# Kernel tuning notes

Hardware: AMD Instinct MI355X
Metric: run time of the kernel (lower is better)

## Reference

```python
import jax, jax.numpy as jnp
import numpy as np
import math

EMBED = 256
NH = 8      # num_heads
NP = 4      # num_points
HD = EMBED // NH  # head_dim = 32
BS = 8
NQ = 8192
HH = 128
WW = 128


def setup_inputs() -> dict:
    key = jax.random.key(0)
    ks = jax.random.split(key, 12)
    query = jax.random.normal(ks[0], (BS, NQ, EMBED), jnp.float32)
    reference_points = jax.random.uniform(ks[1], (BS, NQ, 2), dtype=jnp.float32)
    value = jax.random.normal(ks[2], (BS, HH * WW, EMBED), jnp.float32)
    # sampling_offsets: torch init uses zero weight + structured bias (rose pattern);
    # use small random weight so the math path is exercised, keep the structured bias.
    w_off = 0.001 * jax.random.normal(ks[3], (EMBED, NH * NP * 2), jnp.float32)
    thetas = np.arange(NH, dtype=np.float32) * (2.0 * math.pi / NH)
    grid = np.stack([np.cos(thetas), np.sin(thetas)], -1)          # [NH, 2]
    grid = np.tile(grid[:, None, :], (1, NP, 1)) * np.arange(1, NP + 1, dtype=np.float32)[None, :, None]
    b_off = jnp.asarray(grid.reshape(-1), jnp.float32)              # [NH*NP*2]
    w_attn = 0.01 * jax.random.normal(ks[4], (EMBED, NH * NP), jnp.float32)
    b_attn = jnp.zeros((NH * NP,), jnp.float32)
    xav = 1.0 / math.sqrt(EMBED)
    w_val = xav * jax.random.normal(ks[5], (EMBED, EMBED), jnp.float32)
    b_val = jnp.zeros((EMBED,), jnp.float32)
    w_out = xav * jax.random.normal(ks[6], (EMBED, EMBED), jnp.float32)
    b_out = jnp.zeros((EMBED,), jnp.float32)
    return {"query": query, "reference_points": reference_points, "value": value,
            "w_off": w_off, "b_off": b_off, "w_attn": w_attn, "b_attn": b_attn,
            "w_val": w_val, "b_val": b_val, "w_out": w_out, "b_out": b_out,
            "H": HH, "W": WW}


def _deform_attn(query, reference_points, value, w_off, b_off, w_attn, b_attn,
                 w_val, b_val, w_out, b_out, H, W):
    bs, nq, _ = query.shape
    # value projection -> [bs, nh, H*W, hd]
    v = (value @ w_val + b_val).reshape(bs, H * W, NH, HD).transpose(0, 2, 1, 3)
    # offsets and attention weights
    off = (query @ w_off + b_off).reshape(bs, nq, NH, NP, 2)
    attn = jax.nn.softmax((query @ w_attn + b_attn).reshape(bs, nq, NH, NP), axis=-1)
    norm = jnp.array([W, H], dtype=query.dtype)
    loc = reference_points[:, :, None, None, :] + off / norm       # [bs,nq,nh,np,2] in [0,1]
    # grid_sample, align_corners=False: pixel = loc*size - 0.5  (x <-> W, y <-> H)
    px = (loc[..., 0] * W - 0.5).transpose(0, 2, 1, 3).reshape(bs, NH, nq * NP)
    py = (loc[..., 1] * H - 0.5).transpose(0, 2, 1, 3).reshape(bs, NH, nq * NP)
    x0 = jnp.floor(px); y0 = jnp.floor(py)
    wx = px - x0; wy = py - y0
    x0i = x0.astype(jnp.int32); y0i = y0.astype(jnp.int32)

    def gather(xi, yi):
        # padding_mode='zeros': out-of-range corners contribute 0
        mask = ((xi >= 0) & (xi < W) & (yi >= 0) & (yi < H)).astype(v.dtype)
        idx = jnp.clip(yi, 0, H - 1) * W + jnp.clip(xi, 0, W - 1)   # [bs,nh,K]
        g = jnp.take_along_axis(v, idx[..., None], axis=2)          # [bs,nh,K,hd]
        return g * mask[..., None]

    samp = (((1 - wx) * (1 - wy))[..., None] * gather(x0i, y0i)
            + (wx * (1 - wy))[..., None] * gather(x0i + 1, y0i)
            + ((1 - wx) * wy)[..., None] * gather(x0i, y0i + 1)
            + (wx * wy)[..., None] * gather(x0i + 1, y0i + 1))      # [bs,nh,nq*np,hd]
    samp = samp.reshape(bs, NH, nq, NP, HD)
    aw = attn.transpose(0, 2, 1, 3)                                 # [bs,nh,nq,np]
    out = jnp.einsum('bhqpd,bhqp->bqhd', samp, aw).reshape(bs, nq, EMBED)
    return out @ w_out + b_out


def reference(query, reference_points, value, w_off, b_off, w_attn, b_attn,
              w_val, b_val, w_out, b_out, H, W):
    return _deform_attn(query, reference_points, value, w_off, b_off, w_attn, b_attn,
                        w_val, b_val, w_out, b_out, H, W)
```

## Files before the change

### kernel.cpp

```cpp
#include <hip/hip_runtime.h>
#include <stdint.h>

#define NQ 8192
#define BSZ 8
#define NH 8
#define NP 4
#define HD 32
#define EMBED 256
#define IMG 128
#define NPIX (IMG*IMG)

typedef __attribute__((ext_vector_type(8))) short short8v;
typedef __attribute__((ext_vector_type(4))) float f32x4;

static __device__ __forceinline__ float bf2f(uint32_t u) {
    union { uint32_t i; float f; } x; x.i = u << 16; return x.f;
}
static __device__ __forceinline__ uint16_t f2bf(float f) {
    union { float f; uint32_t i; } x; x.f = f;
    uint32_t r = x.i + 0x7fffu + ((x.i >> 16) & 1u);
    return (uint16_t)(r >> 16);
}
static __device__ __forceinline__ uint32_t cvtpk(float lo, float hi) {
    uint32_t r;
    asm("v_cvt_pk_bf16_f32 %0, %1, %2" : "=v"(r) : "v"(lo), "v"(hi));
    return r;
}
static __device__ __forceinline__ void gload_lds16(const void* g, void* l) {
    __builtin_amdgcn_global_load_lds(
        (const __attribute__((address_space(1))) unsigned int*)g,
        (__attribute__((address_space(3))) unsigned int*)l, 16, 0, 0);
}

#define WAITV(n) asm volatile("s_waitcnt vmcnt(" #n ")" ::: "memory")
#define BARRIER() do { __builtin_amdgcn_s_barrier(); \
                       __builtin_amdgcn_sched_barrier(0); } while (0)

__global__ void pack_w(const float* __restrict__ w_val, const float* __restrict__ w_out,
                       const float* __restrict__ w_off, const float* __restrict__ w_attn,
                       uint16_t* __restrict__ wTval, uint16_t* __restrict__ wTout,
                       uint16_t* __restrict__ wTcat) {
    int k = blockIdx.x;
    int n = threadIdx.x;
    wTval[n * 256 + k] = f2bf(w_val[k * 256 + n]);
    wTout[n * 256 + k] = f2bf(w_out[k * 256 + n]);
    if (n < 64)       wTcat[n * 256 + k]        = f2bf(w_off[k * 64 + n]);
    else if (n < 96)  wTcat[n * 256 + k]        = f2bf(w_attn[k * 32 + (n - 64)]);
}

template<bool A_F32, bool OUT_F32, bool PLANE>
__global__ __launch_bounds__(256, 1)
void gemm_k256(const void* __restrict__ Ap, const uint16_t* __restrict__ BT,
               void* __restrict__ Cp, const float* __restrict__ bias, int M) {
    constexpr int ABYTES = A_F32 ? 16384 : 8192;
    __shared__ char SMEM[131072 + 2 * ABYTES];
    char* Bs = SMEM;
    char* Adbuf[2] = { SMEM + 131072, SMEM + 131072 + ABYTES };
    const int tid = threadIdx.x;
    const int w = tid >> 6, l = tid & 63;
    const int bm = blockIdx.x;
    const int wc = w * 64;

    auto stageA = [&](int buf, int s) {
        const int rowg0 = bm * 64 + s * 16;
        if constexpr (A_F32) {
#pragma unroll
            for (int c = 0; c < 4; ++c) {
                int row = c * 4 + w;
                int x = l * 16;
                const char* src = (const char*)Ap + (size_t)(rowg0 + row) * 1024
                                  + (x ^ ((row & 7) << 4));
                gload_lds16(src, Adbuf[buf] + row * 1024);
            }
        } else {
#pragma unroll
            for (int c = 0; c < 2; ++c) {
                int row2 = (c * 4 + w) * 2;
                int row = row2 + (l >> 5);
                int x = (l & 31) * 16;
                const char* src = (const char*)Ap + (size_t)(rowg0 + row) * 512
                                  + (x ^ ((row & 7) << 4));
                gload_lds16(src, Adbuf[buf] + row2 * 512);
            }
        }
    };

#pragma unroll
    for (int c = 0; c < 32; ++c) {
        int loff = c * 4096 + w * 1024;
        int lofl = loff + l * 16;
        int row = lofl >> 9, x = lofl & 511;
        const char* src = (const char*)BT + (size_t)row * 512 + (x ^ ((row & 7) << 4));
        gload_lds16(src, Bs + loff);
    }
    stageA(0, 0);
    stageA(1, 1);
    if constexpr (A_F32) { WAITV(8); } else { WAITV(4); }
    BARRIER();

    short8v breg[4][8];
#pragma unroll
    for (int n = 0; n < 4; ++n) {
        int col = wc + n * 16 + (l & 15);
        const char* base = Bs + col * 512;
        const int sz = (col & 7) << 4;
#pragma unroll
        for (int k = 0; k < 8; ++k)
            breg[n][k] = *(const short8v*)(base + ((k * 64 + (l >> 4) * 16) ^ sz));
    }

    f32x4 acc[4][4] = {};

#pragma unroll
    for (int s = 0; s < 4; ++s) {
        if (s == 3)              { WAITV(0); }
        else if constexpr (A_F32){ WAITV(4); }
        else                     { WAITV(2); }
        BARRIER();
        const int buf = s & 1;
        short8v a[8];
        const int sz = (l & 7) << 4;
        if constexpr (A_F32) {
            const char* base = Adbuf[buf] + (l & 15) * 1024;
#pragma unroll
            for (int k = 0; k < 8; ++k) {
                int off = k * 128 + (l >> 4) * 32;
                f32x4 lo = *(const f32x4*)(base + (off ^ sz));
                f32x4 hi = *(const f32x4*)(base + ((off + 16) ^ sz));
                union { uint32_t u[4]; short8v s8; } pk;
                pk.u[0] = cvtpk(lo[0], lo[1]); pk.u[1] = cvtpk(lo[2], lo[3]);
                pk.u[2] = cvtpk(hi[0], hi[1]); pk.u[3] = cvtpk(hi[2], hi[3]);
                a[k] = pk.s8;
            }
        } else {
            const char* base = Adbuf[buf] + (l & 15) * 512;
#pragma unroll
            for (int k = 0; k < 8; ++k)
                a[k] = *(const short8v*)(base + ((k * 64 + (l >> 4) * 16) ^ sz));
        }
#pragma unroll
        for (int k = 0; k < 8; ++k)
#pragma unroll
            for (int n = 0; n < 4; ++n)
                acc[s][n] = __builtin_amdgcn_mfma_f32_16x16x32_bf16(a[k], breg[n][k], acc[s][n], 0, 0, 0);
        BARRIER();
        if (s < 2) stageA(buf, s + 2);
    }

    if constexpr (PLANE) {
        uint16_t* Cs = (uint16_t*)(SMEM + 131072);
#pragma unroll
        for (int s = 0; s < 4; ++s)
#pragma unroll
            for (int n = 0; n < 4; ++n) {
                int lcol = wc + n * 16 + (l & 15);
                float bv = bias[lcol];
#pragma unroll
                for (int r = 0; r < 4; ++r) {
                    int lrow = s * 16 + (l >> 4) * 4 + r;
                    *(uint16_t*)((char*)Cs + ((lrow * 512 + lcol * 2) ^ ((lrow & 7) << 4)))
                        = f2bf(acc[s][n][r] + bv);
                }
            }
        __syncthreads();
#pragma unroll
        for (int i = 0; i < 8; ++i) {
            int byteoff = i * 4096 + tid * 16;
            int lrow = byteoff >> 9, x = byteoff & 511;
            uint4 d = *(const uint4*)((const char*)Cs + ((lrow * 512 + x) ^ ((lrow & 7) << 4)));
            int lcol = x >> 1;
            int gr = bm * 64 + lrow;
            int b_ = gr >> 14, pix = gr & 16383;
            int h_ = lcol >> 5, d_ = lcol & 31;
            *(uint4*)((char*)Cp + (((size_t)(b_ * 8 + h_)) << 20) + (size_t)pix * 64 + d_ * 2) = d;
        }
    } else {
#pragma unroll
        for (int s = 0; s < 4; ++s)
#pragma unroll
            for (int n = 0; n < 4; ++n) {
                int col = wc + n * 16 + (l & 15);
                float bv = bias[col];
#pragma unroll
                for (int r = 0; r < 4; ++r) {
                    int gr = bm * 64 + s * 16 + (l >> 4) * 4 + r;
                    float val = acc[s][n][r] + bv;
                    if constexpr (OUT_F32)
                        ((float*)Cp)[(size_t)gr * 256 + col] = val;
                    else
                        ((uint16_t*)Cp)[(size_t)gr * 256 + col] = f2bf(val);
                }
            }
    }
}

__global__ __launch_bounds__(256, 2)
void proj_kernel(const float* __restrict__ Q, const uint16_t* __restrict__ WTcat,
                 const float* __restrict__ b_off, const float* __restrict__ b_attn,
                 const float* __restrict__ refp,
                 float* __restrict__ locs, float* __restrict__ attnw) {
    __shared__ uint16_t Bs[96 * 256];
    __shared__ uint16_t As[64 * 256];
    const int tid = threadIdx.x, w = tid >> 6, l = tid & 63;
    const int blk = blockIdx.x;

#pragma unroll
    for (int c = 0; c < 12; ++c) {
        int loff = (w * 12 + c) * 1024;
        int lofl = loff + l * 16;
        int row = lofl >> 9, colb = lofl & 511;
        const char* src = (const char*)WTcat + (size_t)row * 512 + (colb ^ ((row & 7) << 4));
        gload_lds16(src, (char*)Bs + loff);
    }
#pragma unroll
    for (int c = 0; c < 8; ++c) {
        int loff = tid * 16 + c * 4096;
        int row = loff >> 9, colb = loff & 511;
        const float* src = Q + (size_t)(blk * 64 + row) * 256 + (colb >> 1);
        float4 f0 = *(const float4*)src;
        float4 f1 = *(const float4*)(src + 4);
        uint4 pk;
        pk.x = (uint32_t)f2bf(f0.x) | ((uint32_t)f2bf(f0.y) << 16);
        pk.y = (uint32_t)f2bf(f0.z) | ((uint32_t)f2bf(f0.w) << 16);
        pk.z = (uint32_t)f2bf(f1.x) | ((uint32_t)f2bf(f1.y) << 16);
        pk.w = (uint32_t)f2bf(f1.z) | ((uint32_t)f2bf(f1.w) << 16);
        *(uint4*)((char*)As + row * 512 + (colb ^ ((row & 7) << 4))) = pk;
    }
    __syncthreads();

    f32x4 acc[6] = {};
    const int arow = w * 16 + (l & 15);
#pragma unroll
    for (int ks = 0; ks < 8; ++ks) {
        const int kb = ks * 64 + (l >> 4) * 16;
        short8v a = *(const short8v*)((const char*)As + arow * 512 + (kb ^ ((arow & 7) << 4)));
#pragma unroll
        for (int n = 0; n < 6; ++n) {
            int col = n * 16 + (l & 15);
            short8v b = *(const short8v*)((const char*)Bs + col * 512 + (kb ^ ((col & 7) << 4)));
            acc[n] = __builtin_amdgcn_mfma_f32_16x16x32_bf16(a, b, acc[n], 0, 0, 0);
        }
    }
    __syncthreads();
    float* scores = (float*)As;
#pragma unroll
    for (int n = 0; n < 6; ++n)
#pragma unroll
        for (int r = 0; r < 4; ++r)
            scores[(w * 16 + (l >> 4) * 4 + r) * 96 + n * 16 + (l & 15)] = acc[n][r];
    __syncthreads();

    for (int it = tid; it < 512; it += 256) {
        int row = it >> 3, h = it & 7;
        int gq = blk * 64 + row;
        int b = gq >> 13, q = gq & 8191;
        size_t itemH = ((size_t)(b * 8 + h) << 13) | q;
        float s0 = scores[row * 96 + 64 + h * 4 + 0] + b_attn[h * 4 + 0];
        float s1 = scores[row * 96 + 64 + h * 4 + 1] + b_attn[h * 4 + 1];
        float s2 = scores[row * 96 + 64 + h * 4 + 2] + b_attn[h * 4 + 2];
        float s3 = scores[row * 96 + 64 + h * 4 + 3] + b_attn[h * 4 + 3];
        float mx = fmaxf(fmaxf(s0, s1), fmaxf(s2, s3));
        float e0 = __expf(s0 - mx), e1 = __expf(s1 - mx);
        float e2 = __expf(s2 - mx), e3 = __expf(s3 - mx);
        float inv = 1.0f / (e0 + e1 + e2 + e3);
        float rx = refp[gq * 2 + 0] * 128.0f - 0.5f;
        float ry = refp[gq * 2 + 1] * 128.0f - 0.5f;
        float ew[4] = { e0, e1, e2, e3 };
#pragma unroll
        for (int p = 0; p < 4; ++p) {
            float ox = scores[row * 96 + h * 8 + p * 2 + 0] + b_off[h * 8 + p * 2 + 0];
            float oy = scores[row * 96 + h * 8 + p * 2 + 1] + b_off[h * 8 + p * 2 + 1];
            locs[itemH * 8 + p * 2 + 0] = rx + ox;
            locs[itemH * 8 + p * 2 + 1] = ry + oy;
            attnw[itemH * 4 + p] = ew[p] * inv;
        }
    }
}

__global__ __launch_bounds__(256)
void sample_kernel(const uint16_t* __restrict__ v, const float* __restrict__ locs,
                   const float* __restrict__ attnw, uint16_t* __restrict__ oatt) {
    const int bid = blockIdx.x;
    const int h = bid & 7;
    const int rest = bid >> 3;
    const int b = rest >> 7;
    const int chunk = rest & 127;
    const int qloc = threadIdx.x >> 2;
    const int dg = threadIdx.x & 3;
    const int q = chunk * 64 + qloc;
    const size_t itemH = ((size_t)(b * 8 + h) << 13) | q;
    const char* plane = (const char*)v + ((size_t)(b * 8 + h) << 20);

    float4 l01 = ((const float4*)locs)[itemH * 2 + 0];
    float4 l23 = ((const float4*)locs)[itemH * 2 + 1];
    float4 aw4 = ((const float4*)attnw)[itemH];
    float pxs[4] = { l01.x, l01.z, l23.x, l23.z };
    float pys[4] = { l01.y, l01.w, l23.y, l23.w };
    float aws[4] = { aw4.x, aw4.y, aw4.z, aw4.w };

    float acc[8] = {};
#pragma unroll
    for (int p = 0; p < 4; ++p) {
        float px = pxs[p], py = pys[p], aw = aws[p];
        float fx = floorf(px), fy = floorf(py);
        float wx = px - fx, wy = py - fy;
        int x0 = (int)fx, y0 = (int)fy;
#pragma unroll
        for (int cy = 0; cy < 2; ++cy) {
            int yy = y0 + cy;
            float wyv = cy ? wy : 1.f - wy;
            bool yok = (unsigned)yy < (unsigned)IMG;
            int yc = min(max(yy, 0), IMG - 1);
#pragma unroll
            for (int cx = 0; cx < 2; ++cx) {
                int xx = x0 + cx;
                bool ok = yok && ((unsigned)xx < (unsigned)IMG);
                int xc = min(max(xx, 0), IMG - 1);
                float wgt = ok ? aw * (cx ? wx : 1.f - wx) * wyv : 0.f;
                const uint4 u = *(const uint4*)(plane + ((size_t)(yc * IMG + xc) << 6) + dg * 16);
                acc[0] += wgt * bf2f(u.x & 0xffffu);
                acc[1] += wgt * bf2f(u.x >> 16);
                acc[2] += wgt * bf2f(u.y & 0xffffu);
                acc[3] += wgt * bf2f(u.y >> 16);
                acc[4] += wgt * bf2f(u.z & 0xffffu);
                acc[5] += wgt * bf2f(u.z >> 16);
                acc[6] += wgt * bf2f(u.w & 0xffffu);
                acc[7] += wgt * bf2f(u.w >> 16);
            }
        }
    }
    const size_t bq = (size_t)b * NQ + q;
    uint4 out;
    out.x = (uint32_t)f2bf(acc[0]) | ((uint32_t)f2bf(acc[1]) << 16);
    out.y = (uint32_t)f2bf(acc[2]) | ((uint32_t)f2bf(acc[3]) << 16);
    out.z = (uint32_t)f2bf(acc[4]) | ((uint32_t)f2bf(acc[5]) << 16);
    out.w = (uint32_t)f2bf(acc[6]) | ((uint32_t)f2bf(acc[7]) << 16);
    *(uint4*)((char*)oatt + (bq * 256 + h * 32 + dg * 8) * 2) = out;
}

extern "C" void kernel_launch(void* const* d_in, const int* in_sizes, int n_in,
                              void* d_out, int out_size, void* d_ws, size_t ws_size,
                              hipStream_t stream) {
    const float* query  = (const float*)d_in[0];
    const float* refp   = (const float*)d_in[1];
    const float* value  = (const float*)d_in[2];
    const float* w_off  = (const float*)d_in[3];
    const float* b_off  = (const float*)d_in[4];
    const float* w_attn = (const float*)d_in[5];
    const float* b_attn = (const float*)d_in[6];
    const float* w_val  = (const float*)d_in[7];
    const float* b_val  = (const float*)d_in[8];
    const float* w_out  = (const float*)d_in[9];
    const float* b_out  = (const float*)d_in[10];

    char* ws = (char*)d_ws;
    uint16_t* v     = (uint16_t*)(ws);
    uint16_t* oatt  = (uint16_t*)(ws + 67108864);
    float*    locs  = (float*)(ws + 100663296);
    float*    attnw = (float*)(ws + 117440512);
    uint16_t* wTval = (uint16_t*)(ws + 125829120);
    uint16_t* wTout = (uint16_t*)(ws + 125960192);
    uint16_t* wTcat = (uint16_t*)(ws + 126091264);

    pack_w<<<256, 256, 0, stream>>>(w_val, w_out, w_off, w_attn, wTval, wTout, wTcat);
    gemm_k256<true, false, true><<<2048, 256, 0, stream>>>(value, wTval, v, b_val, 131072);
    proj_kernel<<<1024, 256, 0, stream>>>(query, wTcat, b_off, b_attn, refp, locs, attnw);
    sample_kernel<<<8192, 256, 0, stream>>>(v, locs, attnw, oatt);
    gemm_k256<false, true, false><<<1024, 256, 0, stream>>>(oatt, wTout, (float*)d_out, b_out, 65536);
}
```

Before: 154.9 us.

## Make projection GEMMs persistent over stripes with a deeper A-tile ring buffer

Replaces the one-stripe-per-block GEMM with a 512-thread kernel in which each block handles several 64-row stripes. The 128KB weight tile is loaded into LDS and registers once per block instead of once per stripe. The A-operand pipeline grows from double buffering to a ring with six loads in flight, so global loads overlap MFMA work across stripes. In exchange each block now uses about 160KB of LDS and more registers, so at most one block fits per CU. The grid also becomes 256 blocks, which can leave load imbalance with little room to hide latency.

```diff
diff --git a/kernel.cpp b/kernel.cpp
--- a/kernel.cpp
+++ b/kernel.cpp
@@ -33,8 +33,20 @@
 }
 
 #define WAITV(n) asm volatile("s_waitcnt vmcnt(" #n ")" ::: "memory")
+#define WAITLGKM() do { asm volatile("s_waitcnt lgkmcnt(0)" ::: "memory"); \
+                        __builtin_amdgcn_sched_barrier(0); } while (0)
 #define BARRIER() do { __builtin_amdgcn_s_barrier(); \
                        __builtin_amdgcn_sched_barrier(0); } while (0)
+
+static __device__ __forceinline__ void waitv_n(int n) {
+    switch (n) {
+        case 0: WAITV(0); break;  case 1: WAITV(1); break;
+        case 2: WAITV(2); break;  case 3: WAITV(3); break;
+        case 4: WAITV(4); break;  case 5: WAITV(5); break;
+        case 6: WAITV(6); break;  case 8: WAITV(8); break;
+        default: WAITV(10); break;
+    }
+}
 
 __global__ void pack_w(const float* __restrict__ w_val, const float* __restrict__ w_out,
                        const float* __restrict__ w_off, const float* __restrict__ w_attn,
@@ -48,149 +60,146 @@
     else if (n < 96)  wTcat[n * 256 + k]        = f2bf(w_attn[k * 32 + (n - 64)]);
 }
 
-template<bool A_F32, bool OUT_F32, bool PLANE>
-__global__ __launch_bounds__(256, 1)
-void gemm_k256(const void* __restrict__ Ap, const uint16_t* __restrict__ BT,
-               void* __restrict__ Cp, const float* __restrict__ bias, int M) {
-    constexpr int ABYTES = A_F32 ? 16384 : 8192;
-    __shared__ char SMEM[131072 + 2 * ABYTES];
-    char* Bs = SMEM;
-    char* Adbuf[2] = { SMEM + 131072, SMEM + 131072 + ABYTES };
-    const int tid = threadIdx.x;
-    const int w = tid >> 6, l = tid & 63;
-    const int bm = blockIdx.x;
-    const int wc = w * 64;
-
-    auto stageA = [&](int buf, int s) {
-        const int rowg0 = bm * 64 + s * 16;
+template<bool A_F32, bool OUT_F32, bool PLANE, int STRIPES>
+__global__ __launch_bounds__(512, 2)
+void gemm_pk(const void* __restrict__ Ap, const uint16_t* __restrict__ BT,
+             void* __restrict__ Cp, const float* __restrict__ bias) {
+    constexpr int TILEB = A_F32 ? 16384 : 8192;
+    constexpr int NR    = 131072 / TILEB;
+    constexpr int T     = STRIPES * 4;
+    constexpr int LPT   = A_F32 ? 2 : 1;
+    __shared__ char SMEM[131072 + (PLANE ? 32768 : 0)];
+    char* ring = SMEM;
+    const int tid = threadIdx.x, w = tid >> 6, l = tid & 63;
+    const int stripe0 = blockIdx.x * STRIPES;
+
+    auto stageA = [&](int slot, int t) {
+        const int gr0 = (stripe0 + (t >> 2)) * 64 + (t & 3) * 16;
         if constexpr (A_F32) {
 #pragma unroll
-            for (int c = 0; c < 4; ++c) {
-                int row = c * 4 + w;
-                int x = l * 16;
-                const char* src = (const char*)Ap + (size_t)(rowg0 + row) * 1024
+            for (int c = 0; c < 2; ++c) {
+                int loff = c * 8192 + tid * 16;
+                int row = loff >> 10, x = loff & 1023;
+                const char* src = (const char*)Ap + (size_t)(gr0 + row) * 1024
                                   + (x ^ ((row & 7) << 4));
-                gload_lds16(src, Adbuf[buf] + row * 1024);
+                gload_lds16(src, ring + slot * 16384 + c * 8192 + w * 1024);
             }
         } else {
-#pragma unroll
-            for (int c = 0; c < 2; ++c) {
-                int row2 = (c * 4 + w) * 2;
-                int row = row2 + (l >> 5);
-                int x = (l & 31) * 16;
-                const char* src = (const char*)Ap + (size_t)(rowg0 + row) * 512
-                                  + (x ^ ((row & 7) << 4));
-                gload_lds16(src, Adbuf[buf] + row2 * 512);
-            }
+            int loff = tid * 16;
+            int row = loff >> 9, x = loff & 511;
+            const char* src = (const char*)Ap + (size_t)(gr0 + row) * 512
+                              + (x ^ ((row & 7) << 4));
+            gload_lds16(src, ring + slot * 8192 + w * 1024);
         }
     };
 
 #pragma unroll
-    for (int c = 0; c < 32; ++c) {
-        int loff = c * 4096 + w * 1024;
-        int lofl = loff + l * 16;
-        int row = lofl >> 9, x = lofl & 511;
+    for (int c = 0; c < 16; ++c) {
+        int loff = c * 8192 + tid * 16;
+        int row = loff >> 9, x = loff & 511;
         const char* src = (const char*)BT + (size_t)row * 512 + (x ^ ((row & 7) << 4));
-        gload_lds16(src, Bs + loff);
-    }
-    stageA(0, 0);
-    stageA(1, 1);
-    if constexpr (A_F32) { WAITV(8); } else { WAITV(4); }
+        gload_lds16(src, SMEM + c * 8192 + w * 1024);
+    }
+    WAITV(0);
     BARRIER();
-
-    short8v breg[4][8];
-#pragma unroll
-    for (int n = 0; n < 4; ++n) {
-        int col = wc + n * 16 + (l & 15);
-        const char* base = Bs + col * 512;
+    short8v breg[2][8];
+#pragma unroll
+    for (int n = 0; n < 2; ++n) {
+        int col = w * 32 + n * 16 + (l & 15);
+        const char* base = SMEM + col * 512;
         const int sz = (col & 7) << 4;
 #pragma unroll
         for (int k = 0; k < 8; ++k)
             breg[n][k] = *(const short8v*)(base + ((k * 64 + (l >> 4) * 16) ^ sz));
     }
-
-    f32x4 acc[4][4] = {};
-
-#pragma unroll
-    for (int s = 0; s < 4; ++s) {
-        if (s == 3)              { WAITV(0); }
-        else if constexpr (A_F32){ WAITV(4); }
-        else                     { WAITV(2); }
-        BARRIER();
-        const int buf = s & 1;
-        short8v a[8];
-        const int sz = (l & 7) << 4;
-        if constexpr (A_F32) {
-            const char* base = Adbuf[buf] + (l & 15) * 1024;
-#pragma unroll
-            for (int k = 0; k < 8; ++k) {
-                int off = k * 128 + (l >> 4) * 32;
-                f32x4 lo = *(const f32x4*)(base + (off ^ sz));
-                f32x4 hi = *(const f32x4*)(base + ((off + 16) ^ sz));
-                union { uint32_t u[4]; short8v s8; } pk;
-                pk.u[0] = cvtpk(lo[0], lo[1]); pk.u[1] = cvtpk(lo[2], lo[3]);
-                pk.u[2] = cvtpk(hi[0], hi[1]); pk.u[3] = cvtpk(hi[2], hi[3]);
-                a[k] = pk.s8;
+    WAITLGKM();
+    BARRIER();
+#pragma unroll
+    for (int t = 0; t < 6; ++t) stageA(t & (NR - 1), t);
+
+    for (int st = 0; st < STRIPES; ++st) {
+        f32x4 acc[4][2] = {};
+#pragma unroll
+        for (int s = 0; s < 4; ++s) {
+            const int t = st * 4 + s;
+            const int rem = T - 1 - t;
+            waitv_n((rem < 5 ? rem : 5) * LPT);
+            BARRIER();
+            if (t + 6 < T) stageA((t + 6) & (NR - 1), t + 6);
+            const int slot = t & (NR - 1);
+            short8v a[8];
+            const int sz = (l & 7) << 4;
+            if constexpr (A_F32) {
+                const char* base = ring + slot * 16384 + (l & 15) * 1024;
+#pragma unroll
+                for (int k = 0; k < 8; ++k) {
+                    int off = k * 128 + (l >> 4) * 32;
+                    f32x4 lo = *(const f32x4*)(base + (off ^ sz));
+                    f32x4 hi = *(const f32x4*)(base + ((off + 16) ^ sz));
+                    union { uint32_t u[4]; short8v s8; } pk;
+                    pk.u[0] = cvtpk(lo[0], lo[1]); pk.u[1] = cvtpk(lo[2], lo[3]);
+                    pk.u[2] = cvtpk(hi[0], hi[1]); pk.u[3] = cvtpk(hi[2], hi[3]);
+                    a[k] = pk.s8;
+                }
+            } else {
+                const char* base = ring + slot * 8192 + (l & 15) * 512;
+#pragma unroll
+                for (int k = 0; k < 8; ++k)
+                    a[k] = *(const short8v*)(base + ((k * 64 + (l >> 4) * 16) ^ sz));
+            }
+#pragma unroll
+            for (int k = 0; k < 8; ++k)
+#pragma unroll
+                for (int n = 0; n < 2; ++n)
+                    acc[s][n] = __builtin_amdgcn_mfma_f32_16x16x32_bf16(a[k], breg[n][k], acc[s][n], 0, 0, 0);
+        }
+
+        const int gr0 = (stripe0 + st) * 64;
+        if constexpr (PLANE) {
+            char* Cs = SMEM + 131072;
+#pragma unroll
+            for (int s = 0; s < 4; ++s)
+#pragma unroll
+                for (int n = 0; n < 2; ++n) {
+                    int lcol = w * 32 + n * 16 + (l & 15);
+                    float bv = bias[lcol];
+#pragma unroll
+                    for (int r = 0; r < 4; ++r) {
+                        int lrow = s * 16 + (l >> 4) * 4 + r;
+                        *(uint16_t*)(Cs + ((lrow * 512 + lcol * 2) ^ ((lrow & 7) << 4)))
+                            = f2bf(acc[s][n][r] + bv);
+                    }
+                }
+            WAITLGKM();
+            BARRIER();
+            const int b_ = gr0 >> 14, pix0 = gr0 & 16383;
+            const int hg = tid >> 6, li = tid & 63;
+            char* pb = (char*)Cp + (((size_t)(b_ * 8 + hg)) << 20) + (size_t)pix0 * 64;
+#pragma unroll
+            for (int i = 0; i < 4; ++i) {
+                int fb = i * 1024 + li * 16;
+                int lrow = fb >> 6, x = hg * 64 + (fb & 63);
+                uint4 d = *(const uint4*)(Cs + ((lrow * 512 + x) ^ ((lrow & 7) << 4)));
+                *(uint4*)(pb + (size_t)lrow * 64 + (fb & 63)) = d;
             }
         } else {
-            const char* base = Adbuf[buf] + (l & 15) * 512;
-#pragma unroll
-            for (int k = 0; k < 8; ++k)
-                a[k] = *(const short8v*)(base + ((k * 64 + (l >> 4) * 16) ^ sz));
-        }
-#pragma unroll
-        for (int k = 0; k < 8; ++k)
-#pragma unroll
-            for (int n = 0; n < 4; ++n)
-                acc[s][n] = __builtin_amdgcn_mfma_f32_16x16x32_bf16(a[k], breg[n][k], acc[s][n], 0, 0, 0);
-        BARRIER();
-        if (s < 2) stageA(buf, s + 2);
-    }
-
-    if constexpr (PLANE) {
-        uint16_t* Cs = (uint16_t*)(SMEM + 131072);
-#pragma unroll
-        for (int s = 0; s < 4; ++s)
-#pragma unroll
-            for (int n = 0; n < 4; ++n) {
-                int lcol = wc + n * 16 + (l & 15);
-                float bv = bias[lcol];
-#pragma unroll
-                for (int r = 0; r < 4; ++r) {
-                    int lrow = s * 16 + (l >> 4) * 4 + r;
-                    *(uint16_t*)((char*)Cs + ((lrow * 512 + lcol * 2) ^ ((lrow & 7) << 4)))
-                        = f2bf(acc[s][n][r] + bv);
+#pragma unroll
+            for (int s = 0; s < 4; ++s)
+#pragma unroll
+                for (int n = 0; n < 2; ++n) {
+                    int col = w * 32 + n * 16 + (l & 15);
+                    float bv = bias[col];
+#pragma unroll
+                    for (int r = 0; r < 4; ++r) {
+                        int gr = gr0 + s * 16 + (l >> 4) * 4 + r;
+                        float val = acc[s][n][r] + bv;
+                        if constexpr (OUT_F32)
+                            ((float*)Cp)[(size_t)gr * 256 + col] = val;
+                        else
+                            ((uint16_t*)Cp)[(size_t)gr * 256 + col] = f2bf(val);
+                    }
                 }
-            }
-        __syncthreads();
-#pragma unroll
-        for (int i = 0; i < 8; ++i) {
-            int byteoff = i * 4096 + tid * 16;
-            int lrow = byteoff >> 9, x = byteoff & 511;
-            uint4 d = *(const uint4*)((const char*)Cs + ((lrow * 512 + x) ^ ((lrow & 7) << 4)));
-            int lcol = x >> 1;
-            int gr = bm * 64 + lrow;
-            int b_ = gr >> 14, pix = gr & 16383;
-            int h_ = lcol >> 5, d_ = lcol & 31;
-            *(uint4*)((char*)Cp + (((size_t)(b_ * 8 + h_)) << 20) + (size_t)pix * 64 + d_ * 2) = d;
-        }
-    } else {
-#pragma unroll
-        for (int s = 0; s < 4; ++s)
-#pragma unroll
-            for (int n = 0; n < 4; ++n) {
-                int col = wc + n * 16 + (l & 15);
-                float bv = bias[col];
-#pragma unroll
-                for (int r = 0; r < 4; ++r) {
-                    int gr = bm * 64 + s * 16 + (l >> 4) * 4 + r;
-                    float val = acc[s][n][r] + bv;
-                    if constexpr (OUT_F32)
-                        ((float*)Cp)[(size_t)gr * 256 + col] = val;
-                    else
-                        ((uint16_t*)Cp)[(size_t)gr * 256 + col] = f2bf(val);
-                }
-            }
+        }
     }
 }
 
@@ -363,8 +372,8 @@
     uint16_t* wTcat = (uint16_t*)(ws + 126091264);
 
     pack_w<<<256, 256, 0, stream>>>(w_val, w_out, w_off, w_attn, wTval, wTout, wTcat);
-    gemm_k256<true, false, true><<<2048, 256, 0, stream>>>(value, wTval, v, b_val, 131072);
+    gemm_pk<true, false, true, 8><<<256, 512, 0, stream>>>(value, wTval, v, b_val);
     proj_kernel<<<1024, 256, 0, stream>>>(query, wTcat, b_off, b_attn, refp, locs, attnw);
     sample_kernel<<<8192, 256, 0, stream>>>(v, locs, attnw, oatt);
-    gemm_k256<false, true, false><<<1024, 256, 0, stream>>>(oatt, wTout, (float*)d_out, b_out, 65536);
-}
+    gemm_pk<false, true, false, 4><<<256, 512, 0, stream>>>(oatt, wTout, (float*)d_out, b_out);
+}
```

Result: faster. 140.6 us (-9.2%).
